# Optimization experiments

Hardware: AMD Instinct MI355X
Metric: run time of the kernel (lower is better)

The kernel has to match this reference:

```python
import jax, jax.numpy as jnp
import numpy as np

BIG = 1e10  # stand-in for +inf (no background in a column)


def _edt_2d(mask):
    """Exact Euclidean distance transform of a [H, W] bool mask.
    Returns distance from each True (foreground) pixel to the nearest
    False (background) pixel; 0 at background pixels. Matches
    scipy.ndimage.distance_transform_edt semantics.
    """
    H, W = mask.shape
    idx = jnp.arange(H, dtype=jnp.float32)[:, None]  # [H,1]
    bg = ~mask
    # 1D distance along axis 0 to nearest background in the same column.
    last_bg = jax.lax.cummax(jnp.where(bg, idx, -BIG), axis=0)            # nearest bg above (incl.)
    next_bg = -jax.lax.cummax(jnp.where(bg, -idx, -BIG)[::-1], axis=0)[::-1]  # nearest bg below (incl.)
    g = jnp.minimum(jnp.minimum(idx - last_bg, next_bg - idx), BIG)
    g = jnp.where(mask, g, 0.0)  # [H,W]
    # Separable exact EDT: D^2[i,j] = min_k g[i,k]^2 + (j-k)^2
    j = jnp.arange(W, dtype=jnp.float32)
    offs = (j[:, None] - j[None, :]) ** 2                 # [W,W]
    d2 = jnp.min(g[:, None, :] ** 2 + offs[None, :, :], axis=-1)  # [H,W]
    return jnp.sqrt(d2)


def _distance_field(img2d):
    """field = edt(fg_mask) + edt(bg_mask); zero if no foreground (as in torch code)."""
    fg = img2d > 0.5
    field = _edt_2d(fg) + _edt_2d(~fg)
    return jnp.where(fg.any(), field, 0.0)


def setup_inputs() -> dict:
    key = jax.random.key(0)
    k1, k2 = jax.random.split(key)
    pred = jax.random.uniform(k1, (8, 1, 256, 256), dtype=jnp.float32)
    target = (jax.random.uniform(k2, (8, 1, 256, 256)) > 0.5).astype(jnp.float32)
    return {"pred": pred, "target": target}


def reference(pred, target):
    ALPHA = 2.0
    df = jax.vmap(_distance_field)  # over batch; channel dim is 1
    pred_dt = df(pred[:, 0])[:, None]      # [B,1,H,W]
    target_dt = df(target[:, 0])[:, None]  # [B,1,H,W]
    pred_error = (pred - target) ** 2
    distance = pred_dt ** ALPHA + target_dt ** ALPHA
    return (pred_error * distance).mean()
```

## Files before the change

### kernel.cpp

```cpp
#include <hip/hip_runtime.h>

#define BIG2 1e20f
#define H 256
#define W 256
#define NPIX (H * W)
typedef unsigned long long u64;

__global__ __launch_bounds__(64) void mask_build(
    const float* __restrict__ pred, const float* __restrict__ targ,
    u64* __restrict__ rowmask, int* __restrict__ flags) {
  const int img = blockIdx.x >> 3;
  const int rg = blockIdx.x & 7;
  const int lane = threadIdx.x;
  const float* __restrict__ src =
      (img < 8) ? pred + img * NPIX : targ + (img - 8) * NPIX;
  u64* __restrict__ rm = rowmask + img * 1024;

  u64 anyw = 0;
#pragma unroll 8
  for (int rr = 0; rr < 32; ++rr) {
    const int r = (rg << 5) + rr;
    const u64 w0 = __ballot(src[r * W + lane] > 0.5f);
    const u64 w1 = __ballot(src[r * W + 64 + lane] > 0.5f);
    const u64 w2 = __ballot(src[r * W + 128 + lane] > 0.5f);
    const u64 w3 = __ballot(src[r * W + 192 + lane] > 0.5f);
    anyw |= (w0 | w1 | w2 | w3);
    if (lane == 0) {
      ulonglong2 a; a.x = w0; a.y = w1;
      ulonglong2 b; b.x = w2; b.y = w3;
      ulonglong2* pp = (ulonglong2*)(rm + r * 4);
      pp[0] = a;
      pp[1] = b;
    }
  }
  if (lane == 0 && anyw) atomicOr(&flags[img], 1);
}

__global__ __launch_bounds__(256) void fused_edt_loss(
    const float* __restrict__ pred, const float* __restrict__ targ,
    const u64* __restrict__ rowmask, const int* __restrict__ flags,
    double* __restrict__ partial) {
  const int b = blockIdx.x >> 8;
  const int i = blockIdx.x & (H - 1);
  const int j = threadIdx.x;

  __shared__ u64 mP[H * 4], mT[H * 4];
  __shared__ __align__(16) float gPF[W], gPB[W], gTF[W], gTB[W];
  __shared__ double wsum[4];

  {
    const ulonglong2* gp = (const ulonglong2*)(rowmask + b * 1024);
    const ulonglong2* gt = (const ulonglong2*)(rowmask + (8 + b) * 1024);
    ulonglong2* sp = (ulonglong2*)mP;
    ulonglong2* st = (ulonglong2*)mT;
    sp[j] = gp[j]; sp[j + 256] = gp[j + 256];
    st[j] = gt[j]; st[j + 256] = gt[j + 256];
  }
  const int pix = b * NPIX + i * W + j;
  const float p = pred[pix];
  const float t = targ[pix];
  __syncthreads();

  const int wrd = j >> 6;
  const int sh = j & 63;
  const int clP = (int)((mP[i * 4 + wrd] >> sh) & 1ull);
  const int clT = (int)((mT[i * 4 + wrd] >> sh) & 1ull);

  int dP = 0, dT = 0;
  const int dmax = (i > (H - 1 - i)) ? i : (H - 1 - i);
  for (int d = 1; d <= dmax; ++d) {
    if (__all((dP != 0) & (dT != 0))) break;
    const int iu = i - d, id = i + d;
    if (dP == 0) {
      int f = 0;
      if (iu >= 0) f |= (int)((mP[iu * 4 + wrd] >> sh) & 1ull) ^ clP;
      if (id < H) f |= (int)((mP[id * 4 + wrd] >> sh) & 1ull) ^ clP;
      if (f) dP = d;
    }
    if (dT == 0) {
      int f = 0;
      if (iu >= 0) f |= (int)((mT[iu * 4 + wrd] >> sh) & 1ull) ^ clT;
      if (id < H) f |= (int)((mT[id * 4 + wrd] >> sh) & 1ull) ^ clT;
      if (f) dT = d;
    }
  }
  const float dv2P = dP ? (float)(dP * dP) : BIG2;
  const float dv2T = dT ? (float)(dT * dT) : BIG2;

  gPF[j] = clP ? dv2P : 0.0f;
  gPB[j] = clP ? 0.0f : dv2P;
  gTF[j] = clT ? dv2T : 0.0f;
  gTB[j] = clT ? 0.0f : dv2T;
  __syncthreads();

  const float* __restrict__ baseP = clP ? gPF : gPB;
  const float* __restrict__ baseT = clT ? gTF : gTB;
  float bestP = dv2P, bestT = dv2T;
  for (int d = 1; d < W; ++d) {
    const float dd = (float)(d * d);
    if (__all((dd >= bestP) & (dd >= bestT))) break;
    const int kL = j - d, kR = j + d;
    const int kLc = kL < 0 ? 0 : kL;
    const int kRc = kR > W - 1 ? W - 1 : kR;
    const float cP = fminf(kL >= 0 ? baseP[kLc] : BIG2,
                           kR < W ? baseP[kRc] : BIG2);
    const float cT = fminf(kL >= 0 ? baseT[kLc] : BIG2,
                           kR < W ? baseT[kRc] : BIG2);
    bestP = fminf(bestP, cP + dd);
    bestT = fminf(bestT, cT + dd);
  }

  const float fP = flags[b] ? 1.0f : 0.0f;
  const float fT = flags[8 + b] ? 1.0f : 0.0f;
  const float pe = (p - t) * (p - t);
  double c = (double)(pe * (bestP * fP + bestT * fT));

  for (int off = 32; off > 0; off >>= 1) c += __shfl_down(c, off);
  if ((j & 63) == 0) wsum[j >> 6] = c;
  __syncthreads();
  if (j == 0) partial[blockIdx.x] = wsum[0] + wsum[1] + wsum[2] + wsum[3];
}

__global__ __launch_bounds__(256) void finalize(
    const double* __restrict__ partial, float* __restrict__ out) {
  double s = 0.0;
#pragma unroll
  for (int k = 0; k < 8; ++k) s += partial[threadIdx.x + (k << 8)];
  for (int off = 32; off > 0; off >>= 1) s += __shfl_down(s, off);
  __shared__ double ws[4];
  if ((threadIdx.x & 63) == 0) ws[threadIdx.x >> 6] = s;
  __syncthreads();
  if (threadIdx.x == 0)
    out[0] = (float)((ws[0] + ws[1] + ws[2] + ws[3]) *
                     (1.0 / (8.0 * (double)NPIX)));
}

extern "C" void kernel_launch(void* const* d_in, const int* in_sizes, int n_in,
                              void* d_out, int out_size, void* d_ws,
                              size_t ws_size, hipStream_t stream) {
  const float* pred = (const float*)d_in[0];
  const float* targ = (const float*)d_in[1];
  double* partial = (double*)d_ws;
  int* flags = (int*)((char*)d_ws + 16384);
  u64* rowmask = (u64*)((char*)d_ws + 32768);

  hipMemsetAsync(flags, 0, 64, stream);
  mask_build<<<128, 64, 0, stream>>>(pred, targ, rowmask, flags);
  fused_edt_loss<<<8 * H, 256, 0, stream>>>(pred, targ, rowmask, flags,
                                            partial);
  finalize<<<1, 256, 0, stream>>>(partial, (float*)d_out);
}
```

Before: 79.34 us.

## Compute column distances via bit-transposed masks and fuse finalize into main kernel

The mask is now stored column-major by 64-bit word group. Each wave transposes 64x64 bit blocks with shuffles so every thread holds its column's bits, and finds the nearest opposite-class row with clz/ctz instead of a per-row search loop over shared memory. The separate finalize kernel is removed: the last block, detected with an atomic counter, performs the final reduction. mask_build uses more blocks with a full unroll. Risks are the added shuffle cost of 48 transposes per block and the overhead of last-block detection.

```diff
diff --git a/kernel.cpp b/kernel.cpp
--- a/kernel.cpp
+++ b/kernel.cpp
@@ -8,84 +8,117 @@
 
 __global__ __launch_bounds__(64) void mask_build(
     const float* __restrict__ pred, const float* __restrict__ targ,
-    u64* __restrict__ rowmask, int* __restrict__ flags) {
-  const int img = blockIdx.x >> 3;
-  const int rg = blockIdx.x & 7;
+    u64* __restrict__ rm2, int* __restrict__ flags) {
+  const int img = blockIdx.x >> 4;
+  const int rg = blockIdx.x & 15;
   const int lane = threadIdx.x;
   const float* __restrict__ src =
       (img < 8) ? pred + img * NPIX : targ + (img - 8) * NPIX;
-  u64* __restrict__ rm = rowmask + img * 1024;
+  u64* __restrict__ rm = rm2 + img * 1024;
 
   u64 anyw = 0;
-#pragma unroll 8
-  for (int rr = 0; rr < 32; ++rr) {
-    const int r = (rg << 5) + rr;
+#pragma unroll
+  for (int rr = 0; rr < 16; ++rr) {
+    const int r = (rg << 4) + rr;
     const u64 w0 = __ballot(src[r * W + lane] > 0.5f);
     const u64 w1 = __ballot(src[r * W + 64 + lane] > 0.5f);
     const u64 w2 = __ballot(src[r * W + 128 + lane] > 0.5f);
     const u64 w3 = __ballot(src[r * W + 192 + lane] > 0.5f);
     anyw |= (w0 | w1 | w2 | w3);
     if (lane == 0) {
-      ulonglong2 a; a.x = w0; a.y = w1;
-      ulonglong2 b; b.x = w2; b.y = w3;
-      ulonglong2* pp = (ulonglong2*)(rm + r * 4);
-      pp[0] = a;
-      pp[1] = b;
+      rm[r] = w0; rm[256 + r] = w1; rm[512 + r] = w2; rm[768 + r] = w3;
     }
   }
   if (lane == 0 && anyw) atomicOr(&flags[img], 1);
 }
 
+__device__ __forceinline__ u64 xpose64(u64 x, const int lane) {
+#define XSTEP(S, M)                                                   \
+  {                                                                   \
+    const u64 y = __shfl_xor(x, S, 64);                               \
+    x = (lane & S) ? ((x & (M)) | ((y >> S) & ~(M)))                  \
+                   : ((x & ~(M)) | ((y << S) & (M)));                 \
+  }
+  XSTEP(32, 0xFFFFFFFF00000000ull)
+  XSTEP(16, 0xFFFF0000FFFF0000ull)
+  XSTEP(8, 0xFF00FF00FF00FF00ull)
+  XSTEP(4, 0xF0F0F0F0F0F0F0F0ull)
+  XSTEP(2, 0xCCCCCCCCCCCCCCCCull)
+  XSTEP(1, 0xAAAAAAAAAAAAAAAAull)
+#undef XSTEP
+  return x;
+}
+
 __global__ __launch_bounds__(256) void fused_edt_loss(
     const float* __restrict__ pred, const float* __restrict__ targ,
-    const u64* __restrict__ rowmask, const int* __restrict__ flags,
-    double* __restrict__ partial) {
+    const u64* __restrict__ rm2, const int* __restrict__ flags,
+    double* __restrict__ partial, int* __restrict__ done,
+    float* __restrict__ out) {
   const int b = blockIdx.x >> 8;
   const int i = blockIdx.x & (H - 1);
   const int j = threadIdx.x;
+  const int lane = j & 63;
+  const int w = j >> 6;
 
-  __shared__ u64 mP[H * 4], mT[H * 4];
   __shared__ __align__(16) float gPF[W], gPB[W], gTF[W], gTB[W];
   __shared__ double wsum[4];
+  __shared__ int amLast;
 
-  {
-    const ulonglong2* gp = (const ulonglong2*)(rowmask + b * 1024);
-    const ulonglong2* gt = (const ulonglong2*)(rowmask + (8 + b) * 1024);
-    ulonglong2* sp = (ulonglong2*)mP;
-    ulonglong2* st = (ulonglong2*)mT;
-    sp[j] = gp[j]; sp[j + 256] = gp[j + 256];
-    st[j] = gt[j]; st[j + 256] = gt[j + 256];
-  }
+  const u64* __restrict__ basP = rm2 + b * 1024 + w * 256;
+  const u64* __restrict__ basT = rm2 + (8 + b) * 1024 + w * 256;
+  u64 p0 = basP[lane], p1 = basP[64 + lane], p2 = basP[128 + lane],
+      p3 = basP[192 + lane];
+  u64 t0 = basT[lane], t1 = basT[64 + lane], t2 = basT[128 + lane],
+      t3 = basT[192 + lane];
   const int pix = b * NPIX + i * W + j;
   const float p = pred[pix];
   const float t = targ[pix];
-  __syncthreads();
+  p0 = xpose64(p0, lane); p1 = xpose64(p1, lane);
+  p2 = xpose64(p2, lane); p3 = xpose64(p3, lane);
+  t0 = xpose64(t0, lane); t1 = xpose64(t1, lane);
+  t2 = xpose64(t2, lane); t3 = xpose64(t3, lane);
 
-  const int wrd = j >> 6;
-  const int sh = j & 63;
-  const int clP = (int)((mP[i * 4 + wrd] >> sh) & 1ull);
-  const int clT = (int)((mT[i * 4 + wrd] >> sh) & 1ull);
+  const int gi = i >> 6;
+  const int bb = i & 63;
+  const u64 lm = (~0ull) >> (63 - bb);
+  const u64 hm = (~0ull) << bb;
+  const u64 k0 = gi == 0 ? lm : ~0ull;
+  const u64 k1 = gi < 1 ? 0ull : (gi == 1 ? lm : ~0ull);
+  const u64 k2 = gi < 2 ? 0ull : (gi == 2 ? lm : ~0ull);
+  const u64 k3 = gi < 3 ? 0ull : lm;
+  const u64 q0 = gi > 0 ? 0ull : hm;
+  const u64 q1 = gi > 1 ? 0ull : (gi == 1 ? hm : ~0ull);
+  const u64 q2 = gi > 2 ? 0ull : (gi == 2 ? hm : ~0ull);
+  const u64 q3 = gi == 3 ? hm : ~0ull;
 
-  int dP = 0, dT = 0;
-  const int dmax = (i > (H - 1 - i)) ? i : (H - 1 - i);
-  for (int d = 1; d <= dmax; ++d) {
-    if (__all((dP != 0) & (dT != 0))) break;
-    const int iu = i - d, id = i + d;
-    if (dP == 0) {
-      int f = 0;
-      if (iu >= 0) f |= (int)((mP[iu * 4 + wrd] >> sh) & 1ull) ^ clP;
-      if (id < H) f |= (int)((mP[id * 4 + wrd] >> sh) & 1ull) ^ clP;
-      if (f) dP = d;
-    }
-    if (dT == 0) {
-      int f = 0;
-      if (iu >= 0) f |= (int)((mT[iu * 4 + wrd] >> sh) & 1ull) ^ clT;
-      if (id < H) f |= (int)((mT[id * 4 + wrd] >> sh) & 1ull) ^ clT;
-      if (f) dT = d;
-    }
+#define VDIST(c0, c1, c2, c3, CL, DV2)                                \
+  {                                                                   \
+    const u64 cw = gi == 0 ? c0 : gi == 1 ? c1 : gi == 2 ? c2 : c3;   \
+    CL = (int)((cw >> bb) & 1ull);                                    \
+    const u64 inv = CL ? ~0ull : 0ull;                                \
+    const u64 o0 = c0 ^ inv, o1 = c1 ^ inv, o2 = c2 ^ inv,            \
+              o3 = c3 ^ inv;                                          \
+    const u64 u0 = o0 & k0, u1 = o1 & k1, u2 = o2 & k2, u3 = o3 & k3; \
+    int last = -30000;                                                \
+    if (u0) last = 63 - __builtin_clzll(u0);                          \
+    if (u1) last = 127 - __builtin_clzll(u1);                         \
+    if (u2) last = 191 - __builtin_clzll(u2);                         \
+    if (u3) last = 255 - __builtin_clzll(u3);                         \
+    const u64 d0 = o0 & q0, d1 = o1 & q1, d2 = o2 & q2, d3 = o3 & q3; \
+    int nxt = 30000;                                                  \
+    if (d3) nxt = 192 + __builtin_ctzll(d3);                          \
+    if (d2) nxt = 128 + __builtin_ctzll(d2);                          \
+    if (d1) nxt = 64 + __builtin_ctzll(d1);                           \
+    if (d0) nxt = __builtin_ctzll(d0);                                \
+    const int up = i - last, dn = nxt - i;                            \
+    const int dv = up < dn ? up : dn;                                 \
+    DV2 = (dv >= 1000) ? BIG2 : (float)(dv * dv);                     \
   }
-  const float dv2P = dP ? (float)(dP * dP) : BIG2;
-  const float dv2T = dT ? (float)(dT * dT) : BIG2;
+  int clP, clT;
+  float dv2P, dv2T;
+  VDIST(p0, p1, p2, p3, clP, dv2P)
+  VDIST(t0, t1, t2, t3, clT, dv2T)
+#undef VDIST
 
   gPF[j] = clP ? dv2P : 0.0f;
   gPB[j] = clP ? 0.0f : dv2P;
@@ -114,25 +147,28 @@
   const float fT = flags[8 + b] ? 1.0f : 0.0f;
   const float pe = (p - t) * (p - t);
   double c = (double)(pe * (bestP * fP + bestT * fT));
-
   for (int off = 32; off > 0; off >>= 1) c += __shfl_down(c, off);
   if ((j & 63) == 0) wsum[j >> 6] = c;
   __syncthreads();
-  if (j == 0) partial[blockIdx.x] = wsum[0] + wsum[1] + wsum[2] + wsum[3];
-}
+  if (j == 0) {
+    partial[blockIdx.x] = wsum[0] + wsum[1] + wsum[2] + wsum[3];
+    __threadfence();
+    amLast = (atomicAdd(done, 1) == (int)gridDim.x - 1);
+  }
+  __syncthreads();
 
-__global__ __launch_bounds__(256) void finalize(
-    const double* __restrict__ partial, float* __restrict__ out) {
-  double s = 0.0;
+  if (amLast) {
+    __threadfence();
+    double s = 0.0;
 #pragma unroll
-  for (int k = 0; k < 8; ++k) s += partial[threadIdx.x + (k << 8)];
-  for (int off = 32; off > 0; off >>= 1) s += __shfl_down(s, off);
-  __shared__ double ws[4];
-  if ((threadIdx.x & 63) == 0) ws[threadIdx.x >> 6] = s;
-  __syncthreads();
-  if (threadIdx.x == 0)
-    out[0] = (float)((ws[0] + ws[1] + ws[2] + ws[3]) *
-                     (1.0 / (8.0 * (double)NPIX)));
+    for (int k = 0; k < 8; ++k) s += partial[j + (k << 8)];
+    for (int off = 32; off > 0; off >>= 1) s += __shfl_down(s, off);
+    if ((j & 63) == 0) wsum[j >> 6] = s;
+    __syncthreads();
+    if (j == 0)
+      out[0] = (float)((wsum[0] + wsum[1] + wsum[2] + wsum[3]) *
+                       (1.0 / (8.0 * (double)NPIX)));
+  }
 }
 
 extern "C" void kernel_launch(void* const* d_in, const int* in_sizes, int n_in,
@@ -142,11 +178,11 @@
   const float* targ = (const float*)d_in[1];
   double* partial = (double*)d_ws;
   int* flags = (int*)((char*)d_ws + 16384);
-  u64* rowmask = (u64*)((char*)d_ws + 32768);
+  int* done = (int*)((char*)d_ws + 16448);
+  u64* rm2 = (u64*)((char*)d_ws + 32768);
 
-  hipMemsetAsync(flags, 0, 64, stream);
-  mask_build<<<128, 64, 0, stream>>>(pred, targ, rowmask, flags);
-  fused_edt_loss<<<8 * H, 256, 0, stream>>>(pred, targ, rowmask, flags,
-                                            partial);
-  finalize<<<1, 256, 0, stream>>>(partial, (float*)d_out);
+  hipMemsetAsync(flags, 0, 128, stream);
+  mask_build<<<256, 64, 0, stream>>>(pred, targ, rm2, flags);
+  fused_edt_loss<<<8 * H, 256, 0, stream>>>(pred, targ, rm2, flags, partial,
+                                            done, (float*)d_out);
 }
```

After: 110.0 us. +38.6%, slower.
